# Kernel optimization log

Measured on AMD Instinct MI355X. Metric: run time of the kernel, lower is better.

## Reference

```python
import jax, jax.numpy as jnp
import numpy as np

THETA = 10000.0
D_K = 128
MAX_SEQ_LEN = 4096
BATCH, N_HEADS, SEQ_LEN = 4, 16, 4096


def build_ro_weights(theta, d_k, max_seq_len, dtype=jnp.float32):
    # Block-diagonal 2x2 rotation matrices, identical math to the torch loop.
    k = jnp.arange(d_k // 2, dtype=dtype)                      # [d_k/2]
    pos = jnp.arange(max_seq_len, dtype=dtype)                 # [S]
    inv_freq = theta ** (-2.0 * k / d_k)                       # [d_k/2]
    ang = pos[:, None] * inv_freq[None, :]                     # [S, d_k/2]
    cos, sin = jnp.cos(ang), jnp.sin(ang)
    ev = 2 * jnp.arange(d_k // 2)
    od = ev + 1
    R = jnp.zeros((max_seq_len, d_k, d_k), dtype=dtype)
    R = R.at[:, ev, ev].set(cos)
    R = R.at[:, ev, od].set(-sin)
    R = R.at[:, od, ev].set(sin)
    R = R.at[:, od, od].set(cos)
    return R


def setup_inputs() -> dict:
    key = jax.random.key(0)
    kx, = jax.random.split(key, 1)
    x = jax.random.normal(kx, (BATCH, N_HEADS, SEQ_LEN, D_K), dtype=jnp.float32)
    token_positions = jnp.arange(SEQ_LEN, dtype=jnp.int64 if jax.config.jax_enable_x64 else jnp.int32)
    ro_weights = build_ro_weights(THETA, D_K, MAX_SEQ_LEN)
    return {"x": x, "token_positions": token_positions, "ro_weights": ro_weights}


def reference(x, token_positions, ro_weights):
    # Gather per-position rotation matrices, then batched matvec:
    # out[..., s, i] = sum_j ro_weights[pos[s], i, j] * x[..., s, j]
    R = ro_weights[token_positions]                # [S, d_k, d_k]
    return jnp.einsum('...sj,sij->...si', x, R)
```

## Files before the change

### kernel.cpp

```cpp
#include <hip/hip_runtime.h>
#include <hip/hip_bf16.h>
#include <math.h>


#define ROPE_D     128
#define ROPE_S     4096
#define ROPE_N4    (4*16*4096*32)
#define ROWS_PER_B 32
#define F4_PER_B   1024
#define NEG_L2T_64 (-0.20762050593046012f)

__global__ __launch_bounds__(256) void
RotaryPositionalEmbedding_68332929679843_kernel(const float* __restrict__ x,
                                                const int* __restrict__ pos,
                                                float* __restrict__ out) {
    __shared__ float cs[ROWS_PER_B][ROPE_D];

    const int t = threadIdx.x;
    const int row0 = blockIdx.x * ROWS_PER_B;

#pragma unroll
    for (int i = 0; i < 8; ++i) {
        const int pairIdx = t + 256 * i;
        const int r = pairIdx >> 6;
        const int k = pairIdx & 63;
        const int s = (row0 + r) & (ROPE_S - 1);
        const float p = (float)pos[s];
        const float invf = exp2f((float)k * NEG_L2T_64);
        const float ang = p * invf;
        float sv, cv;
        sincosf(ang, &sv, &cv);
        cs[r][k] = cv;
        cs[r][64 + k] = sv;
    }
    __syncthreads();

    const int base = blockIdx.x * F4_PER_B + t;
#pragma unroll
    for (int it = 0; it < 4; ++it) {
        const int i4 = base + it * 256;
        const int r  = (i4 >> 5) & (ROWS_PER_B - 1);
        const int c4 = i4 & 31;
        const int k  = c4 * 2;

        const float4 v = *(const float4*)(x + (size_t)i4 * 4);
        const float c0 = cs[r][k],     s0 = cs[r][64 + k];
        const float c1 = cs[r][k + 1], s1 = cs[r][64 + k + 1];

        float4 o;
        o.x = c0 * v.x - s0 * v.y;
        o.y = s0 * v.x + c0 * v.y;
        o.z = c1 * v.z - s1 * v.w;
        o.w = s1 * v.z + c1 * v.w;
        *(float4*)(out + (size_t)i4 * 4) = o;
    }
}

extern "C" void kernel_launch(void* const* d_in, const int* in_sizes, int n_in,
                              void* d_out, int out_size, void* d_ws, size_t ws_size,
                              hipStream_t stream) {
    const float* x   = (const float*)d_in[0];
    const int*   tp  = (const int*)d_in[1];
    float*       out = (float*)d_out;

    RotaryPositionalEmbedding_68332929679843_kernel<<<dim3(ROPE_N4 / F4_PER_B),
                                                      dim3(256), 0, stream>>>(x, tp, out);
}
```

Before: 411.9 us.

## Precompute cos/sin table in workspace and apply with nontemporal vector loads

Splits the kernel in two. A small pre-pass writes a per-position cos/sin table into the workspace, and the apply kernel reads that table (2 MB, likely cache-resident) in place of recomputing sincos per block, with no shared memory or barrier. The apply kernel also streams x and out with nontemporal loads and stores. This adds a second launch and a dependency on the workspace being large enough, falling back to the old kernel otherwise.

Measured after the change: 403.7 us. -2.0%, faster.

```diff
diff --git a/kernel.cpp b/kernel.cpp
--- a/kernel.cpp
+++ b/kernel.cpp
@@ -1,24 +1,62 @@
 #include <hip/hip_runtime.h>
-#include <hip/hip_bf16.h>
 #include <math.h>
 
+
+typedef float v4f __attribute__((ext_vector_type(4)));
 
 #define ROPE_D     128
 #define ROPE_S     4096
 #define ROPE_N4    (4*16*4096*32)
+#define F4_PER_B   1024
+#define TAB_N4     (ROPE_S*32)
+#define NEG_L2T_64 (-0.20762050593046012f)
+
+__global__ __launch_bounds__(256) void
+rope_build_table_68332929679843(const int* __restrict__ pos,
+                                v4f* __restrict__ tab) {
+    const int idx = blockIdx.x * 256 + threadIdx.x;
+    const int s   = idx >> 5;
+    const int c4  = idx & 31;
+    const float p = (float)pos[s];
+    const int k   = c4 * 2;
+    const float invf0 = exp2f((float)k       * NEG_L2T_64);
+    const float invf1 = exp2f((float)(k + 1) * NEG_L2T_64);
+    float s0, c0, s1, c1;
+    sincosf(p * invf0, &s0, &c0);
+    sincosf(p * invf1, &s1, &c1);
+    v4f t;
+    t.x = c0; t.y = s0; t.z = c1; t.w = s1;
+    tab[idx] = t;
+}
+
+__global__ __launch_bounds__(256) void
+rope_apply_68332929679843(const v4f* __restrict__ x,
+                          const v4f* __restrict__ tab,
+                          v4f* __restrict__ out) {
+    const int base = blockIdx.x * F4_PER_B + threadIdx.x;
+#pragma unroll
+    for (int it = 0; it < 4; ++it) {
+        const int i4 = base + it * 256;
+        const v4f t = tab[i4 & (TAB_N4 - 1)];
+        const v4f v = __builtin_nontemporal_load(&x[i4]);
+        v4f o;
+        o.x = t.x * v.x - t.y * v.y;
+        o.y = t.y * v.x + t.x * v.y;
+        o.z = t.z * v.z - t.w * v.w;
+        o.w = t.w * v.z + t.z * v.w;
+        __builtin_nontemporal_store(o, &out[i4]);
+    }
+}
+
 #define ROWS_PER_B 32
-#define F4_PER_B   1024
-#define NEG_L2T_64 (-0.20762050593046012f)
 
 __global__ __launch_bounds__(256) void
 RotaryPositionalEmbedding_68332929679843_kernel(const float* __restrict__ x,
                                                 const int* __restrict__ pos,
                                                 float* __restrict__ out) {
     __shared__ float cs[ROWS_PER_B][ROPE_D];
-
     const int t = threadIdx.x;
     const int row0 = blockIdx.x * ROWS_PER_B;
-
 #pragma unroll
     for (int i = 0; i < 8; ++i) {
         const int pairIdx = t + 256 * i;
@@ -34,7 +72,6 @@
         cs[r][64 + k] = sv;
     }
     __syncthreads();
-
     const int base = blockIdx.x * F4_PER_B + t;
 #pragma unroll
     for (int it = 0; it < 4; ++it) {
@@ -42,11 +79,9 @@
         const int r  = (i4 >> 5) & (ROWS_PER_B - 1);
         const int c4 = i4 & 31;
         const int k  = c4 * 2;
-
         const float4 v = *(const float4*)(x + (size_t)i4 * 4);
         const float c0 = cs[r][k],     s0 = cs[r][64 + k];
         const float c1 = cs[r][k + 1], s1 = cs[r][64 + k + 1];
-
         float4 o;
         o.x = c0 * v.x - s0 * v.y;
         o.y = s0 * v.x + c0 * v.y;
@@ -63,6 +98,13 @@
     const int*   tp  = (const int*)d_in[1];
     float*       out = (float*)d_out;
 
-    RotaryPositionalEmbedding_68332929679843_kernel<<<dim3(ROPE_N4 / F4_PER_B),
-                                                      dim3(256), 0, stream>>>(x, tp, out);
+    if (ws_size >= (size_t)TAB_N4 * sizeof(v4f)) {
+        v4f* tab = (v4f*)d_ws;
+        rope_build_table_68332929679843<<<dim3(TAB_N4 / 256), dim3(256), 0, stream>>>(tp, tab);
+        rope_apply_68332929679843<<<dim3(ROPE_N4 / F4_PER_B), dim3(256), 0, stream>>>(
+            (const v4f*)x, tab, (v4f*)out);
+    } else {
+        RotaryPositionalEmbedding_68332929679843_kernel<<<dim3(ROPE_N4 / F4_PER_B),
+                                                          dim3(256), 0, stream>>>(x, tp, out);
+    }
 }
```

## Compute rotation per thread once and reuse across sixteen batch-head slices

Applied to the files above, without the earlier changes.

Each thread computes the cos/sin for its column pair once in registers and applies them to the same position across 16 batch-head slices, removing the shared-memory table and the block barrier. Loads and stores use nontemporal builtins and are batched four at a time to raise memory-level parallelism. This cuts trig work sixteenfold but adds strided accesses spaced by a full head, and the grid has fewer blocks.

After: 404.7 us, median of 2. About the same (-1.8%).

```diff
diff --git a/kernel.cpp b/kernel.cpp
--- a/kernel.cpp
+++ b/kernel.cpp
@@ -1,68 +1,67 @@
 #include <hip/hip_runtime.h>
-#include <hip/hip_bf16.h>
 #include <math.h>
 
 
-#define ROPE_D     128
+typedef float v4f __attribute__((ext_vector_type(4)));
+
 #define ROPE_S     4096
-#define ROPE_N4    (4*16*4096*32)
-#define ROWS_PER_B 32
-#define F4_PER_B   1024
+#define TAB_N4     (ROPE_S*32)
+#define NBH        64
+#define SLICES     16
+#define NTHREADS   (TAB_N4*(NBH/SLICES))
 #define NEG_L2T_64 (-0.20762050593046012f)
 
 __global__ __launch_bounds__(256) void
-RotaryPositionalEmbedding_68332929679843_kernel(const float* __restrict__ x,
+RotaryPositionalEmbedding_68332929679843_kernel(const v4f* __restrict__ x,
                                                 const int* __restrict__ pos,
-                                                float* __restrict__ out) {
-    __shared__ float cs[ROWS_PER_B][ROPE_D];
+                                                v4f* __restrict__ out) {
+    const int g   = blockIdx.x * 256 + threadIdx.x;
+    const int tab = g & (TAB_N4 - 1);
+    const int bh0 = (g >> 17) * SLICES;
+    const int s   = tab >> 5;
+    const int c4  = tab & 31;
 
-    const int t = threadIdx.x;
-    const int row0 = blockIdx.x * ROWS_PER_B;
+    const float p = (float)pos[s];
+    const int k   = c4 * 2;
+    const float invf0 = exp2f((float)k       * NEG_L2T_64);
+    const float invf1 = exp2f((float)(k + 1) * NEG_L2T_64);
+    float s0, c0, s1, c1;
+    sincosf(p * invf0, &s0, &c0);
+    sincosf(p * invf1, &s1, &c1);
+
+    const size_t base = (size_t)bh0 * TAB_N4 + (size_t)tab;
 
 #pragma unroll
-    for (int i = 0; i < 8; ++i) {
-        const int pairIdx = t + 256 * i;
-        const int r = pairIdx >> 6;
-        const int k = pairIdx & 63;
-        const int s = (row0 + r) & (ROPE_S - 1);
-        const float p = (float)pos[s];
-        const float invf = exp2f((float)k * NEG_L2T_64);
-        const float ang = p * invf;
-        float sv, cv;
-        sincosf(ang, &sv, &cv);
-        cs[r][k] = cv;
-        cs[r][64 + k] = sv;
-    }
-    __syncthreads();
+    for (int j = 0; j < SLICES; j += 4) {
+        v4f v0 = __builtin_nontemporal_load(&x[base + (size_t)(j + 0) * TAB_N4]);
+        v4f v1 = __builtin_nontemporal_load(&x[base + (size_t)(j + 1) * TAB_N4]);
+        v4f v2 = __builtin_nontemporal_load(&x[base + (size_t)(j + 2) * TAB_N4]);
+        v4f v3 = __builtin_nontemporal_load(&x[base + (size_t)(j + 3) * TAB_N4]);
 
-    const int base = blockIdx.x * F4_PER_B + t;
-#pragma unroll
-    for (int it = 0; it < 4; ++it) {
-        const int i4 = base + it * 256;
-        const int r  = (i4 >> 5) & (ROWS_PER_B - 1);
-        const int c4 = i4 & 31;
-        const int k  = c4 * 2;
+        v4f o0, o1, o2, o3;
+        o0.x = c0 * v0.x - s0 * v0.y;  o0.y = s0 * v0.x + c0 * v0.y;
+        o0.z = c1 * v0.z - s1 * v0.w;  o0.w = s1 * v0.z + c1 * v0.w;
+        o1.x = c0 * v1.x - s0 * v1.y;  o1.y = s0 * v1.x + c0 * v1.y;
+        o1.z = c1 * v1.z - s1 * v1.w;  o1.w = s1 * v1.z + c1 * v1.w;
+        o2.x = c0 * v2.x - s0 * v2.y;  o2.y = s0 * v2.x + c0 * v2.y;
+        o2.z = c1 * v2.z - s1 * v2.w;  o2.w = s1 * v2.z + c1 * v2.w;
+        o3.x = c0 * v3.x - s0 * v3.y;  o3.y = s0 * v3.x + c0 * v3.y;
+        o3.z = c1 * v3.z - s1 * v3.w;  o3.w = s1 * v3.z + c1 * v3.w;
 
-        const float4 v = *(const float4*)(x + (size_t)i4 * 4);
-        const float c0 = cs[r][k],     s0 = cs[r][64 + k];
-        const float c1 = cs[r][k + 1], s1 = cs[r][64 + k + 1];
-
-        float4 o;
-        o.x = c0 * v.x - s0 * v.y;
-        o.y = s0 * v.x + c0 * v.y;
-        o.z = c1 * v.z - s1 * v.w;
-        o.w = s1 * v.z + c1 * v.w;
-        *(float4*)(out + (size_t)i4 * 4) = o;
+        __builtin_nontemporal_store(o0, &out[base + (size_t)(j + 0) * TAB_N4]);
+        __builtin_nontemporal_store(o1, &out[base + (size_t)(j + 1) * TAB_N4]);
+        __builtin_nontemporal_store(o2, &out[base + (size_t)(j + 2) * TAB_N4]);
+        __builtin_nontemporal_store(o3, &out[base + (size_t)(j + 3) * TAB_N4]);
     }
 }
 
 extern "C" void kernel_launch(void* const* d_in, const int* in_sizes, int n_in,
                               void* d_out, int out_size, void* d_ws, size_t ws_size,
                               hipStream_t stream) {
-    const float* x   = (const float*)d_in[0];
-    const int*   tp  = (const int*)d_in[1];
-    float*       out = (float*)d_out;
+    const v4f* x   = (const v4f*)d_in[0];
+    const int* tp  = (const int*)d_in[1];
+    v4f*       out = (v4f*)d_out;
 
-    RotaryPositionalEmbedding_68332929679843_kernel<<<dim3(ROPE_N4 / F4_PER_B),
+    RotaryPositionalEmbedding_68332929679843_kernel<<<dim3(NTHREADS / 256),
                                                       dim3(256), 0, stream>>>(x, tp, out);
 }
```
